# Kernel tuning notes

Hardware: AMD Instinct MI355X
Metric: run time of the kernel (lower is better)

The kernel has to match this reference:

```python
import jax, jax.numpy as jnp
import numpy as np

B, L, M = 256, 8, 1024  # batch, input_length (= window), latent dim m
P = 8                   # predict_length


def setup_inputs() -> dict:
    key = jax.random.key(0)
    k1, k2, k3 = jax.random.split(key, 3)
    x = jax.random.normal(k1, (B, L, M), dtype=jnp.float32)
    # A initialized near identity (original init is torch.eye repeated), plus
    # small noise so the test is non-trivial and the recurrence stays stable.
    eye = jnp.broadcast_to(jnp.eye(M, dtype=jnp.float32), (L, M, M))
    A_real = eye / L + 0.02 * jax.random.normal(k2, (L, M, M), dtype=jnp.float32)
    A_imag = 0.02 * jax.random.normal(k3, (L, M, M), dtype=jnp.float32)
    return {"x": x, "A_real": A_real, "A_imag": A_imag, "predict_length": P}


def reference(x, A_real, A_imag, predict_length):
    # Complex DMD operator bank: A[j] is [M, M] cfloat.
    A = (A_real + 1j * A_imag).astype(jnp.complex64)
    Lw = x.shape[1]
    # Original inner loop: u2 += A[j] @ uc[:, -j]  (note -0 == 0!)
    #   j=0 pairs A[0] with window position 0; j>=1 pairs A[j] with position Lw-j.
    # Re-index so term for window position p uses Ag[p]: Ag[0]=A[0], Ag[p]=A[Lw-p].
    idx = jnp.concatenate([jnp.array([0]), jnp.arange(Lw - 1, 0, -1)])
    Ag = A[idx]  # [Lw, M, M]

    uc0 = x.astype(jnp.complex64)  # [B, Lw, M] sliding window state

    def step(uc, _):
        # Fused accumulation: sum_p Ag[p] @ uc[:, p]  -> [B, M]
        u2 = jnp.einsum("kmn,bkn->bm", Ag, uc)
        uc = jnp.concatenate([uc[:, 1:], u2[:, None]], axis=1)  # slide window
        return uc, None

    uc, _ = jax.lax.scan(step, uc0, None, length=predict_length)
    # Original casts cfloat -> double, which drops the imaginary part; keep fp32.
    return jnp.real(uc).astype(jnp.float32)
```

## Files before the change

kernel.cpp:

```cpp
#include <hip/hip_runtime.h>


#define LW 8

typedef __attribute__((ext_vector_type(8))) short  short8;
typedef __attribute__((ext_vector_type(8))) __bf16 bf16x8;
typedef __attribute__((ext_vector_type(4))) float  f32x4;
typedef __attribute__((ext_vector_type(4))) float  f4;
typedef const __attribute__((address_space(1))) void gvoid_t;
typedef __attribute__((address_space(3))) void lvoid_t;

static __device__ __forceinline__ short f2bf(float f) {
  unsigned u = __builtin_bit_cast(unsigned, f);
  u += 0x7FFFu + ((u >> 16) & 1u);
  return (short)(u >> 16);
}
static __device__ __forceinline__ float bf2f(short s) {
  unsigned u = ((unsigned)(unsigned short)s) << 16;
  return __builtin_bit_cast(float, u);
}
static __device__ __forceinline__ f32x4 mfma16(short8 a, short8 b, f32x4 c) {
  return __builtin_amdgcn_mfma_f32_16x16x32_bf16(
      __builtin_bit_cast(bf16x8, a), __builtin_bit_cast(bf16x8, b), c, 0, 0, 0);
}

__global__ __launch_bounds__(1024) void prep_all(const float* __restrict__ x,
                                                 const float* __restrict__ Ar,
                                                 const float* __restrict__ Ai,
                                                 short* __restrict__ Sr2,
                                                 short* __restrict__ Si2,
                                                 short* __restrict__ Wr5,
                                                 short* __restrict__ Wi5) {
  const int bid = blockIdx.x;
  if (bid < 1024) {
    const int tg = bid * 1024 + threadIdx.x;
    const int sq = tg & 3, col = (tg >> 2) & 31, kcg = (tg >> 7) & 31;
    const int colt = (tg >> 12) & 31, p = tg >> 17;
    const int qn = sq ^ ((col >> 1) & 3);
    const int m = (colt << 5) + col, n0 = (kcg << 5) + (qn << 3);
    const int qm = (LW - p) & 7;
    const size_t src = ((size_t)((qm << 10) + m) << 10) + n0;
    f4 r0 = *(const f4*)(Ar + src), r1 = *(const f4*)(Ar + src + 4);
    f4 i0 = *(const f4*)(Ai + src), i1 = *(const f4*)(Ai + src + 4);
    short8 vr, vi;
#pragma unroll
    for (int j = 0; j < 4; ++j) {
      vr[j] = f2bf(r0[j]); vr[j + 4] = f2bf(r1[j]);
      vi[j] = f2bf(i0[j]); vi[j + 4] = f2bf(i1[j]);
    }
    *(short8*)(Wr5 + ((size_t)tg << 3)) = vr;
    *(short8*)(Wi5 + ((size_t)tg << 3)) = vi;
  } else {
    const int tg = (bid - 1024) * 1024 + threadIdx.x;
    const int qn = tg & 3, kc = (tg >> 2) & 31, b = (tg >> 7) & 255, s = tg >> 15;
    const float* xp = x + ((size_t)(b * LW + s) << 10) + (kc << 5) + (qn << 3);
    f4 x0 = *(const f4*)xp, x1 = *(const f4*)(xp + 4);
    short8 v;
#pragma unroll
    for (int j = 0; j < 4; ++j) { v[j] = f2bf(x0[j]); v[j + 4] = f2bf(x1[j]); }
    const int sq = qn ^ ((b >> 1) & 3);
    const size_t dst = ((size_t)s << 18) + (kc << 13) + (b << 5) + (sq << 3);
    *(short8*)(Sr2 + dst) = v;
    short8 z = {0, 0, 0, 0, 0, 0, 0, 0};
    *(short8*)(Si2 + dst) = z;
  }
}


#define LOADA(set_, kc_) do {                                                    \
    const int kg_ = ((ks << 4) + (kc_)) << 13;                                   \
    _Pragma("unroll")                                                            \
    for (int rf_ = 0; rf_ < 4; ++rf_) {                                          \
      aR[set_][rf_] = *(const short8*)(SrB + kg_ + aoffG[rf_]);                  \
      aI[set_][rf_] = *(const short8*)(SiB + kg_ + aoffG[rf_]);                  \
    }                                                                            \
  } while (0)

#define LOADA_R(set_, kc_) do {                                                  \
    const int kg_ = ((ks << 4) + (kc_)) << 13;                                   \
    _Pragma("unroll")                                                            \
    for (int rf_ = 0; rf_ < 4; ++rf_) {                                          \
      aR[set_][rf_] = *(const short8*)(SrB + kg_ + aoffG[rf_]);                  \
    }                                                                            \
  } while (0)

#define LOADB(set_, kc_) do {                                                    \
    _Pragma("unroll")                                                            \
    for (int cf_ = 0; cf_ < 2; ++cf_) {                                          \
      bRp[set_][cf_] = *(const short8*)(ldsW + ((kc_) << 10) + boffL[cf_]);      \
      bIp[set_][cf_] = *(const short8*)(ldsW + 16384 + ((kc_) << 10) + boffL[cf_]); \
    }                                                                            \
  } while (0)

#define COMP(aset_, bset_) do {                                                  \
    __builtin_amdgcn_s_setprio(1);                                               \
    _Pragma("unroll")                                                            \
    for (int rf_ = 0; rf_ < 4; ++rf_) {                                          \
      const short8 nI_ = aI[aset_][rf_] ^ SGN;                                   \
      _Pragma("unroll")                                                          \
      for (int cf_ = 0; cf_ < 2; ++cf_) {                                        \
        accR[rf_][cf_] = mfma16(aR[aset_][rf_], bRp[bset_][cf_], accR[rf_][cf_]); \
        accR[rf_][cf_] = mfma16(nI_,            bIp[bset_][cf_], accR[rf_][cf_]); \
        accI[rf_][cf_] = mfma16(aR[aset_][rf_], bIp[bset_][cf_], accI[rf_][cf_]); \
        accI[rf_][cf_] = mfma16(aI[aset_][rf_], bRp[bset_][cf_], accI[rf_][cf_]); \
      }                                                                          \
    }                                                                            \
    __builtin_amdgcn_s_setprio(0);                                               \
  } while (0)

#define COMP_LIGHT(aset_, bset_) do {                                            \
    __builtin_amdgcn_s_setprio(1);                                               \
    _Pragma("unroll")                                                            \
    for (int rf_ = 0; rf_ < 4; ++rf_) {                                          \
      _Pragma("unroll")                                                          \
      for (int cf_ = 0; cf_ < 2; ++cf_) {                                        \
        accR[rf_][cf_] = mfma16(aR[aset_][rf_], bRp[bset_][cf_], accR[rf_][cf_]); \
        accI[rf_][cf_] = mfma16(aR[aset_][rf_], bIp[bset_][cf_], accI[rf_][cf_]); \
      }                                                                          \
    }                                                                            \
    __builtin_amdgcn_s_setprio(0);                                               \
  } while (0)

#define COMP_R(aset_, bset_) do {                                                \
    __builtin_amdgcn_s_setprio(1);                                               \
    _Pragma("unroll")                                                            \
    for (int rf_ = 0; rf_ < 4; ++rf_) {                                          \
      const short8 nI_ = aI[aset_][rf_] ^ SGN;                                   \
      _Pragma("unroll")                                                          \
      for (int cf_ = 0; cf_ < 2; ++cf_) {                                        \
        accR[rf_][cf_] = mfma16(aR[aset_][rf_], bRp[bset_][cf_], accR[rf_][cf_]); \
        accR[rf_][cf_] = mfma16(nI_,            bIp[bset_][cf_], accR[rf_][cf_]); \
      }                                                                          \
    }                                                                            \
    __builtin_amdgcn_s_setprio(0);                                               \
  } while (0)

#define COMP_LIGHT_R(aset_, bset_) do {                                          \
    __builtin_amdgcn_s_setprio(1);                                               \
    _Pragma("unroll")                                                            \
    for (int rf_ = 0; rf_ < 4; ++rf_) {                                          \
      _Pragma("unroll")                                                          \
      for (int cf_ = 0; cf_ < 2; ++cf_) {                                        \
        accR[rf_][cf_] = mfma16(aR[aset_][rf_], bRp[bset_][cf_], accR[rf_][cf_]); \
      }                                                                          \
    }                                                                            \
    __builtin_amdgcn_s_setprio(0);                                               \
  } while (0)

#define KLOOP(LAP_, CMP_) do {                                                   \
    LAP_(0, 0);                                                                  \
    LAP_(1, 1);                                                                  \
    __syncthreads();                 \
    LOADB(0, 0);                                                                 \
    _Pragma("unroll")                                                            \
    for (int kc = 0; kc < 16; ++kc) {                                            \
      if (kc < 14) LAP_((kc + 2) % 3, kc + 2);                                   \
      if (kc < 15) LOADB((kc + 1) & 1, kc + 1);                                  \
      CMP_(kc % 3, kc & 1);                                                      \
    }                                                                            \
  } while (0)

__global__ __launch_bounds__(256, 2) void gemm_step(const short* __restrict__ Sr2,
                                                    const short* __restrict__ Si2,
                                                    const short* __restrict__ Wr5,
                                                    const short* __restrict__ Wi5,
                                                    short* __restrict__ Pp,
                                                    int t) {
  __shared__ short ldsW[32768];

  const int bid   = blockIdx.x;
  const int inner = bid >> 3;
  const int colt  = inner & 31;
  const int ks    = inner >> 5;
  const int p     = (bid & 7) ^ (ks << 2);
  const int s     = (p + t) & 7;

  const int tid = threadIdx.x, lane = tid & 63, w = tid >> 6;
  const int l15 = lane & 15, q = lane >> 4;

  {
    const short* baseR = Wr5 + (((size_t)((p << 5) + colt)) << 15) + ((size_t)ks << 14);
    const short* baseI = Wi5 + (((size_t)((p << 5) + colt)) << 15) + ((size_t)ks << 14);
#pragma unroll
    for (int j = 0; j < 16; ++j) {
      const int gid  = (j << 8) + tid;
      const int arr  = gid >> 11;
      const int rem  = gid & 2047;
      const short* src = (arr ? baseI : baseR) + (rem << 3);
      __builtin_amdgcn_global_load_lds((gvoid_t*)src,
          (lvoid_t*)&ldsW[(arr << 14) + (rem << 3)], 16, 0, 0);
    }
  }

  const short* SrB = Sr2 + ((size_t)s << 18);
  const short* SiB = Si2 + ((size_t)s << 18);
  int aoffG[4], boffL[2];
#pragma unroll
  for (int rf = 0; rf < 4; ++rf) {
    const int row = (w << 6) + (rf << 4) + l15;
    aoffG[rf] = (row << 5) + ((q ^ ((row >> 1) & 3)) << 3);
  }
#pragma unroll
  for (int cf = 0; cf < 2; ++cf) {
    const int col = (cf << 4) + l15;
    boffL[cf] = (col << 5) + ((q ^ ((col >> 1) & 3)) << 3);
  }

  f32x4 accR[4][2], accI[4][2];
  const f32x4 z4 = {0.f, 0.f, 0.f, 0.f};
#pragma unroll
  for (int a = 0; a < 4; ++a)
#pragma unroll
    for (int c = 0; c < 2; ++c) { accR[a][c] = z4; accI[a][c] = z4; }

  const short8 SGN = {(short)0x8000, (short)0x8000, (short)0x8000, (short)0x8000,
                      (short)0x8000, (short)0x8000, (short)0x8000, (short)0x8000};

  short8 aR[3][4], aI[3][4];
  short8 bRp[2][2], bIp[2][2];

  if (t != 7) {
    if (s >= t) KLOOP(LOADA_R, COMP_LIGHT);
    else        KLOOP(LOADA,   COMP);
  } else {
    if (s == 7) KLOOP(LOADA_R, COMP_LIGHT_R);
    else        KLOOP(LOADA,   COMP_R);
  }

  short* op = Pp + ((size_t)(((((p << 1) + ks) << 5) + colt) << 3) << 11) + (tid << 3);
#pragma unroll
  for (int rf = 0; rf < 4; ++rf)
#pragma unroll
    for (int cf = 0; cf < 2; ++cf) {
      short8 sv;
#pragma unroll
      for (int rg = 0; rg < 4; ++rg) {
        sv[rg]     = f2bf(accR[rf][cf][rg]);
        sv[rg + 4] = f2bf(accI[rf][cf][rg]);
      }
      *(short8*)(op + ((size_t)((rf << 1) + cf) << 11)) = sv;
    }
}

__global__ __launch_bounds__(512) void reduce_step(const short* __restrict__ Pp,
                                                   short* __restrict__ Sr2,
                                                   short* __restrict__ Si2,
                                                   float* __restrict__ out,
                                                   int t) {
  const int r    = blockIdx.x * 512 + threadIdx.x;
  const int half = r & 1;
  const int g    = r >> 1;
  const int tidg = g & 255, o = (g >> 8) & 7, colt = g >> 11;

  float sum[8] = {0.f, 0.f, 0.f, 0.f, 0.f, 0.f, 0.f, 0.f};
  const int sl0 = half << 3;
#pragma unroll
  for (int si = 0; si < 8; ++si) {
    const int sl = sl0 + si;
    const short8 v = *(const short8*)(
        Pp + ((size_t)((((sl << 5) + colt) << 3) + o) << 11) + (tidg << 3));
#pragma unroll
    for (int jj = 0; jj < 8; ++jj) sum[jj] += bf2f(v[jj]);
  }

#pragma unroll
  for (int jj = 0; jj < 8; ++jj) sum[jj] += __shfl_xor(sum[jj], 1);

  if (half == 0) {
    const int rf = o >> 1, cf = o & 1;
    const int lane = tidg & 63, w = tidg >> 6;
    const int l15 = lane & 15, q = lane >> 4;
    const int row0 = (w << 6) + (rf << 4) + (q << 2);
    const int col  = (colt << 5) + (cf << 4) + l15;
    const int kc = col >> 5, qn = (col >> 3) & 3, j = col & 7;

#pragma unroll
    for (int rg = 0; rg < 4; ++rg) {
      const int row = row0 + rg;
      out[((size_t)((row << 3) + t) << 10) + col] = sum[rg];
      if (t != 7) {
        const int sq = qn ^ ((row >> 1) & 3);
        const size_t idx = ((size_t)t << 18) + (kc << 13) + (row << 5) + (sq << 3) + j;
        Sr2[idx] = f2bf(sum[rg]);
        Si2[idx] = f2bf(sum[rg + 4]);
      }
    }
  }
}

extern "C" void kernel_launch(void* const* d_in, const int* in_sizes, int n_in,
                              void* d_out, int out_size, void* d_ws, size_t ws_size,
                              hipStream_t stream) {
  const float* x  = (const float*)d_in[0];
  const float* Ar = (const float*)d_in[1];
  const float* Ai = (const float*)d_in[2];
  float* out = (float*)d_out;

  char* ws = (char*)d_ws;
  if (ws_size < (60u << 20)) return;
  short* Sr2 = (short*)(ws);
  short* Si2 = (short*)(ws + (4u  << 20));
  short* Wr5 = (short*)(ws + (8u  << 20));
  short* Wi5 = (short*)(ws + (24u << 20));
  short* Pp  = (short*)(ws + (40u << 20));

  prep_all<<<dim3(1280), dim3(1024), 0, stream>>>(x, Ar, Ai, Sr2, Si2, Wr5, Wi5);
  for (int t = 0; t < 8; ++t) {
    gemm_step<<<dim3(512), dim3(256), 0, stream>>>(Sr2, Si2, Wr5, Wi5, Pp, t);
    reduce_step<<<dim3(256), dim3(512), 0, stream>>>(Pp, Sr2, Si2, out, t);
  }
}
```

Measured before the change: 208.7 us.

## Precompute all input-only partial products in one batched kernel before recurrence

The partial GEMMs that touch only the original input window (real-only state, s >= t) are hoisted out of the sequential step loop into a single large pre_light launch covering all 36 (t,p) combinations. Each step's gemm_heavy then early-exits for those blocks and computes only the complex terms that depend on earlier outputs. The t=0 step skips the heavy launch entirely. The input state is replicated 8 times so concurrent blocks spread their reads, and partial products are kept per step in a larger workspace. The cost is a much larger workspace requirement, extra replication writes, and half-empty heavy launches.

```diff
diff --git a/kernel.cpp b/kernel.cpp
--- a/kernel.cpp
+++ b/kernel.cpp
@@ -30,7 +30,8 @@
                                                  short* __restrict__ Sr2,
                                                  short* __restrict__ Si2,
                                                  short* __restrict__ Wr5,
-                                                 short* __restrict__ Wi5) {
+                                                 short* __restrict__ Wi5,
+                                                 short* __restrict__ SrRep) {
   const int bid = blockIdx.x;
   if (bid < 1024) {
     const int tg = bid * 1024 + threadIdx.x;
@@ -63,9 +64,11 @@
     *(short8*)(Sr2 + dst) = v;
     short8 z = {0, 0, 0, 0, 0, 0, 0, 0};
     *(short8*)(Si2 + dst) = z;
+#pragma unroll
+    for (int r = 0; r < 8; ++r)
+      *(short8*)(SrRep + ((size_t)r << 21) + dst) = v;
   }
 }
-
 
 #define LOADA(set_, kc_) do {                                                    \
     const int kg_ = ((ks << 4) + (kc_)) << 13;                                   \
@@ -135,22 +138,10 @@
     __builtin_amdgcn_s_setprio(0);                                               \
   } while (0)
 
-#define COMP_LIGHT_R(aset_, bset_) do {                                          \
-    __builtin_amdgcn_s_setprio(1);                                               \
-    _Pragma("unroll")                                                            \
-    for (int rf_ = 0; rf_ < 4; ++rf_) {                                          \
-      _Pragma("unroll")                                                          \
-      for (int cf_ = 0; cf_ < 2; ++cf_) {                                        \
-        accR[rf_][cf_] = mfma16(aR[aset_][rf_], bRp[bset_][cf_], accR[rf_][cf_]); \
-      }                                                                          \
-    }                                                                            \
-    __builtin_amdgcn_s_setprio(0);                                               \
-  } while (0)
-
 #define KLOOP(LAP_, CMP_) do {                                                   \
     LAP_(0, 0);                                                                  \
     LAP_(1, 1);                                                                  \
-    __syncthreads();                 \
+    __syncthreads();                                        \
     LOADB(0, 0);                                                                 \
     _Pragma("unroll")                                                            \
     for (int kc = 0; kc < 16; ++kc) {                                            \
@@ -160,12 +151,98 @@
     }                                                                            \
   } while (0)
 
-__global__ __launch_bounds__(256, 2) void gemm_step(const short* __restrict__ Sr2,
-                                                    const short* __restrict__ Si2,
+#define WLOAD() do {                                                             \
+    const short* baseR = Wr5 + (((size_t)((p << 5) + colt)) << 15) + ((size_t)ks << 14); \
+    const short* baseI = Wi5 + (((size_t)((p << 5) + colt)) << 15) + ((size_t)ks << 14); \
+    _Pragma("unroll")                                                            \
+    for (int j = 0; j < 16; ++j) {                                               \
+      const int gid  = (j << 8) + tid;                                           \
+      const int arr  = gid >> 11;                                                \
+      const int rem  = gid & 2047;                                               \
+      const short* src = (arr ? baseI : baseR) + (rem << 3);                     \
+      __builtin_amdgcn_global_load_lds((gvoid_t*)src,                            \
+          (lvoid_t*)&ldsW[(arr << 14) + (rem << 3)], 16, 0, 0);                  \
+    }                                                                            \
+  } while (0)
+
+#define OFFSETS() do {                                                           \
+    _Pragma("unroll")                                                            \
+    for (int rf = 0; rf < 4; ++rf) {                                             \
+      const int row = (w << 6) + (rf << 4) + l15;                                \
+      aoffG[rf] = (row << 5) + ((q ^ ((row >> 1) & 3)) << 3);                    \
+    }                                                                            \
+    _Pragma("unroll")                                                            \
+    for (int cf = 0; cf < 2; ++cf) {                                             \
+      const int col = (cf << 4) + l15;                                           \
+      boffL[cf] = (col << 5) + ((q ^ ((col >> 1) & 3)) << 3);                    \
+    }                                                                            \
+  } while (0)
+
+#define STOREP(PpT_) do {                                                        \
+    short* op = (PpT_) + ((size_t)(((((p << 1) + ks) << 5) + colt) << 3) << 11) + (tid << 3); \
+    _Pragma("unroll")                                                            \
+    for (int rf = 0; rf < 4; ++rf)                                               \
+      _Pragma("unroll")                                                          \
+      for (int cf = 0; cf < 2; ++cf) {                                           \
+        short8 sv;                                                               \
+        _Pragma("unroll")                                                        \
+        for (int rg = 0; rg < 4; ++rg) {                                         \
+          sv[rg]     = f2bf(accR[rf][cf][rg]);                                   \
+          sv[rg + 4] = f2bf(accI[rf][cf][rg]);                                   \
+        }                                                                        \
+        *(short8*)(op + ((size_t)((rf << 1) + cf) << 11)) = sv;                  \
+      }                                                                          \
+  } while (0)
+
+__global__ __launch_bounds__(256, 2) void pre_light(const short* __restrict__ SrRep,
                                                     const short* __restrict__ Wr5,
                                                     const short* __restrict__ Wi5,
-                                                    short* __restrict__ Pp,
-                                                    int t) {
+                                                    short* __restrict__ Pp) {
+  __shared__ short ldsW[32768];
+
+  const int bid   = blockIdx.x;
+  const int u     = bid >> 6;
+  const int inner = bid & 63;
+  const int colt  = inner & 31;
+  const int ks    = inner >> 5;
+
+  const int cum[9] = {0, 8, 15, 21, 26, 30, 33, 35, 36};
+  int t = 7;
+#pragma unroll
+  for (int tt = 0; tt < 8; ++tt) if (u >= cum[tt] && u < cum[tt + 1]) t = tt;
+  const int p = u - cum[t];
+  const int s = p + t;
+
+  const int tid = threadIdx.x, lane = tid & 63, w = tid >> 6;
+  const int l15 = lane & 15, q = lane >> 4;
+
+  WLOAD();
+
+  const short* SrB = SrRep + ((size_t)(bid & 7) << 21) + ((size_t)s << 18);
+  int aoffG[4], boffL[2];
+  OFFSETS();
+
+  f32x4 accR[4][2], accI[4][2];
+  const f32x4 z4 = {0.f, 0.f, 0.f, 0.f};
+#pragma unroll
+  for (int a = 0; a < 4; ++a)
+#pragma unroll
+    for (int c = 0; c < 2; ++c) { accR[a][c] = z4; accI[a][c] = z4; }
+
+  short8 aR[3][4];
+  short8 bRp[2][2], bIp[2][2];
+
+  KLOOP(LOADA_R, COMP_LIGHT);
+
+  STOREP(Pp + ((size_t)t << 23));
+}
+
+__global__ __launch_bounds__(256, 2) void gemm_heavy(const short* __restrict__ Sr2,
+                                                     const short* __restrict__ Si2,
+                                                     const short* __restrict__ Wr5,
+                                                     const short* __restrict__ Wi5,
+                                                     short* __restrict__ Pp,
+                                                     int t) {
   __shared__ short ldsW[32768];
 
   const int bid   = blockIdx.x;
@@ -175,36 +252,17 @@
   const int p     = (bid & 7) ^ (ks << 2);
   const int s     = (p + t) & 7;
 
+  if (s >= t) return;
+
   const int tid = threadIdx.x, lane = tid & 63, w = tid >> 6;
   const int l15 = lane & 15, q = lane >> 4;
 
-  {
-    const short* baseR = Wr5 + (((size_t)((p << 5) + colt)) << 15) + ((size_t)ks << 14);
-    const short* baseI = Wi5 + (((size_t)((p << 5) + colt)) << 15) + ((size_t)ks << 14);
-#pragma unroll
-    for (int j = 0; j < 16; ++j) {
-      const int gid  = (j << 8) + tid;
-      const int arr  = gid >> 11;
-      const int rem  = gid & 2047;
-      const short* src = (arr ? baseI : baseR) + (rem << 3);
-      __builtin_amdgcn_global_load_lds((gvoid_t*)src,
-          (lvoid_t*)&ldsW[(arr << 14) + (rem << 3)], 16, 0, 0);
-    }
-  }
+  WLOAD();
 
   const short* SrB = Sr2 + ((size_t)s << 18);
   const short* SiB = Si2 + ((size_t)s << 18);
   int aoffG[4], boffL[2];
-#pragma unroll
-  for (int rf = 0; rf < 4; ++rf) {
-    const int row = (w << 6) + (rf << 4) + l15;
-    aoffG[rf] = (row << 5) + ((q ^ ((row >> 1) & 3)) << 3);
-  }
-#pragma unroll
-  for (int cf = 0; cf < 2; ++cf) {
-    const int col = (cf << 4) + l15;
-    boffL[cf] = (col << 5) + ((q ^ ((col >> 1) & 3)) << 3);
-  }
+  OFFSETS();
 
   f32x4 accR[4][2], accI[4][2];
   const f32x4 z4 = {0.f, 0.f, 0.f, 0.f};
@@ -219,27 +277,10 @@
   short8 aR[3][4], aI[3][4];
   short8 bRp[2][2], bIp[2][2];
 
-  if (t != 7) {
-    if (s >= t) KLOOP(LOADA_R, COMP_LIGHT);
-    else        KLOOP(LOADA,   COMP);
-  } else {
-    if (s == 7) KLOOP(LOADA_R, COMP_LIGHT_R);
-    else        KLOOP(LOADA,   COMP_R);
-  }
-
-  short* op = Pp + ((size_t)(((((p << 1) + ks) << 5) + colt) << 3) << 11) + (tid << 3);
-#pragma unroll
-  for (int rf = 0; rf < 4; ++rf)
-#pragma unroll
-    for (int cf = 0; cf < 2; ++cf) {
-      short8 sv;
-#pragma unroll
-      for (int rg = 0; rg < 4; ++rg) {
-        sv[rg]     = f2bf(accR[rf][cf][rg]);
-        sv[rg + 4] = f2bf(accI[rf][cf][rg]);
-      }
-      *(short8*)(op + ((size_t)((rf << 1) + cf) << 11)) = sv;
-    }
+  if (t != 7) KLOOP(LOADA, COMP);
+  else        KLOOP(LOADA, COMP_R);
+
+  STOREP(Pp + ((size_t)t << 23));
 }
 
 __global__ __launch_bounds__(512) void reduce_step(const short* __restrict__ Pp,
@@ -247,6 +288,7 @@
                                                    short* __restrict__ Si2,
                                                    float* __restrict__ out,
                                                    int t) {
+  const short* PpT = Pp + ((size_t)t << 23);
   const int r    = blockIdx.x * 512 + threadIdx.x;
   const int half = r & 1;
   const int g    = r >> 1;
@@ -258,7 +300,7 @@
   for (int si = 0; si < 8; ++si) {
     const int sl = sl0 + si;
     const short8 v = *(const short8*)(
-        Pp + ((size_t)((((sl << 5) + colt) << 3) + o) << 11) + (tidg << 3));
+        PpT + ((size_t)((((sl << 5) + colt) << 3) + o) << 11) + (tidg << 3));
 #pragma unroll
     for (int jj = 0; jj < 8; ++jj) sum[jj] += bf2f(v[jj]);
   }
@@ -297,16 +339,19 @@
   float* out = (float*)d_out;
 
   char* ws = (char*)d_ws;
-  if (ws_size < (60u << 20)) return;
-  short* Sr2 = (short*)(ws);
-  short* Si2 = (short*)(ws + (4u  << 20));
-  short* Wr5 = (short*)(ws + (8u  << 20));
-  short* Wi5 = (short*)(ws + (24u << 20));
-  short* Pp  = (short*)(ws + (40u << 20));
-
-  prep_all<<<dim3(1280), dim3(1024), 0, stream>>>(x, Ar, Ai, Sr2, Si2, Wr5, Wi5);
+  if (ws_size < (200u << 20)) return;
+  short* Sr2   = (short*)(ws);
+  short* Si2   = (short*)(ws + (4u  << 20));
+  short* Wr5   = (short*)(ws + (8u  << 20));
+  short* Wi5   = (short*)(ws + (24u << 20));
+  short* SrRep = (short*)(ws + (40u << 20));
+  short* Pp    = (short*)(ws + (72u << 20));
+
+  prep_all<<<dim3(1280), dim3(1024), 0, stream>>>(x, Ar, Ai, Sr2, Si2, Wr5, Wi5, SrRep);
+  pre_light<<<dim3(2304), dim3(256), 0, stream>>>(SrRep, Wr5, Wi5, Pp);
   for (int t = 0; t < 8; ++t) {
-    gemm_step<<<dim3(512), dim3(256), 0, stream>>>(Sr2, Si2, Wr5, Wi5, Pp, t);
+    if (t > 0)
+      gemm_heavy<<<dim3(512), dim3(256), 0, stream>>>(Sr2, Si2, Wr5, Wi5, Pp, t);
     reduce_step<<<dim3(256), dim3(512), 0, stream>>>(Pp, Sr2, Si2, out, t);
   }
 }
```

Measured after the change: 252.4 us. 20.9% more time.
